# Optimization experiments

Hardware: AMD Instinct MI355X
Metric: run time of the kernel (lower is better)

## Reference

```python
import jax, jax.numpy as jnp
import numpy as np

N = 2          # batch (upsample scale for sample i is i+1, shapes chosen so no crop occurs)
C = 512        # channels for both branches
TH = TW = 256  # target H,W taken from pts_feats[0]
IMG_SIZES = [128, 64, 32, 16, 8]  # 5-level FPN
BN_EPS = 1e-5


def setup_inputs() -> dict:
    key = jax.random.key(0)
    ks = jax.random.split(key, 24)
    inp = {}
    for l, s in enumerate(IMG_SIZES):
        inp[f'img_feat{l}'] = jax.random.normal(ks[l], (N, C, s, s), jnp.float32)
    inp['pts_feat0'] = jax.random.normal(ks[5], (N, C, TH, TW), jnp.float32)
    # 1x1 conv + BN params (eval-mode BN with running stats)
    inp['img_w'] = jax.random.normal(ks[6], (C, C), jnp.float32) * 0.02
    inp['img_b'] = jax.random.normal(ks[7], (C,), jnp.float32) * 0.02
    inp['img_gamma'] = jnp.ones((C,), jnp.float32)
    inp['img_beta'] = jnp.zeros((C,), jnp.float32)
    inp['img_mean'] = jnp.zeros((C,), jnp.float32)
    inp['img_var'] = jax.random.uniform(ks[8], (C,), jnp.float32, 0.5, 1.5)
    inp['pts_w'] = jax.random.normal(ks[9], (C, C), jnp.float32) * 0.02
    inp['pts_b'] = jax.random.normal(ks[10], (C,), jnp.float32) * 0.02
    inp['pts_gamma'] = jnp.ones((C,), jnp.float32)
    inp['pts_beta'] = jnp.zeros((C,), jnp.float32)
    inp['pts_mean'] = jnp.zeros((C,), jnp.float32)
    inp['pts_var'] = jax.random.uniform(ks[11], (C,), jnp.float32, 0.5, 1.5)
    return inp


def _obtain_mlvl(feats, th, tw):
    # Faithful to original: per-sample loop (scale_factor depends on batch index,
    # so each sample has a different static upsampled shape -> Python loop over N=2).
    n = feats[0].shape[0]
    outs = []
    for i in range(n):
        acc = None
        for lvl, f in enumerate(feats):
            x = f[i]  # [C, h, w]
            if lvl > 0:
                s = i + 1  # nearest upsample by batch-index+1 (as in source)
                x = jnp.repeat(jnp.repeat(x, s, axis=1), s, axis=2)
            dh = th - x.shape[1]
            dw = tw - x.shape[2]
            x = jnp.pad(x, ((0, 0), (dh // 2, dh - dh // 2), (dw // 2, dw - dw // 2)), mode='edge')
            acc = x if acc is None else acc + x
        outs.append(acc)
    return jnp.stack(outs, 0)  # [N, C, th, tw]


def _conv_bn_relu(x, w, b, gamma, beta, mean, var):
    # 1x1 conv == channel contraction, then eval-mode BN, then ReLU
    y = jnp.einsum('nchw,oc->nohw', x, w) + b[None, :, None, None]
    scale = gamma / jnp.sqrt(var + BN_EPS)
    y = (y - mean[None, :, None, None]) * scale[None, :, None, None] + beta[None, :, None, None]
    return jax.nn.relu(y)


def reference(img_feat0, img_feat1, img_feat2, img_feat3, img_feat4, pts_feat0,
              img_w, img_b, img_gamma, img_beta, img_mean, img_var,
              pts_w, pts_b, pts_gamma, pts_beta, pts_mean, pts_var):
    th, tw = pts_feat0.shape[2], pts_feat0.shape[3]
    pts_m = _obtain_mlvl([pts_feat0], th, tw)  # pts_levels=1
    pts_pre = _conv_bn_relu(pts_m, pts_w, pts_b, pts_gamma, pts_beta, pts_mean, pts_var)
    img_m = _obtain_mlvl([img_feat0, img_feat1, img_feat2, img_feat3, img_feat4], th, tw)
    img_pre = _conv_bn_relu(img_m, img_w, img_b, img_gamma, img_beta, img_mean, img_var)
    # dropout is identity in eval mode (deterministic reference)
    return jnp.concatenate((img_pre, pts_pre), axis=1)  # [N, 2C, th, tw]
```

## Files before the change

### kernel.cpp

```cpp
#include <hip/hip_runtime.h>

typedef unsigned short u16;
typedef __attribute__((ext_vector_type(8))) short s8frag;
typedef __attribute__((ext_vector_type(4))) float f32x4;

#define GLOAD16(gp, lp)                                                        \
  __builtin_amdgcn_global_load_lds(                                            \
      (const __attribute__((address_space(1))) void*)(gp),                     \
      (__attribute__((address_space(3))) void*)(lp), 16, 0, 0)

__device__ __forceinline__ u16 f2bf(float x) {
  unsigned int u = __float_as_uint(x);
  unsigned int r = (u + 0x7fffu + ((u >> 16) & 1u)) >> 16;
  return (u16)r;
}

__global__ __launch_bounds__(256) void prep_w(
    const float* __restrict__ wi, const float* __restrict__ bi,
    const float* __restrict__ gi, const float* __restrict__ bei,
    const float* __restrict__ mi, const float* __restrict__ vi,
    const float* __restrict__ wp, const float* __restrict__ bp,
    const float* __restrict__ gp, const float* __restrict__ bep,
    const float* __restrict__ mp, const float* __restrict__ vp,
    u16* __restrict__ wout_i, float* __restrict__ bias_i,
    u16* __restrict__ wout_p, float* __restrict__ bias_p) {
  int gidx = blockIdx.x * 256 + threadIdx.x;
  int branch = gidx >> 18;
  int idx = gidx & ((1 << 18) - 1);
  int o = idx >> 9, c = idx & 511;
  const float* w = branch ? wp : wi;
  const float* b = branch ? bp : bi;
  const float* g = branch ? gp : gi;
  const float* be = branch ? bep : bei;
  const float* mn = branch ? mp : mi;
  const float* vr = branch ? vp : vi;
  u16* wo = branch ? wout_p : wout_i;
  float* bo = branch ? bias_p : bias_i;
  float scale = g[o] * rsqrtf(vr[o] + 1e-5f);
  wo[idx] = f2bf(w[idx] * scale);
  if (c == 0) bo[o] = scale * (b[o] - mn[o]) + be[o];
}

__global__ __launch_bounds__(256) void build_b(
    const float* __restrict__ f0, const float* __restrict__ f1,
    const float* __restrict__ f2, const float* __restrict__ f3,
    const float* __restrict__ f4, const float* __restrict__ pts,
    u16* __restrict__ Bimg, u16* __restrict__ Bpts) {
  __shared__ float tile[64][65];
  int t = threadIdx.x;
  int wblk = blockIdx.x;
  int h = blockIdx.y;
  int z = blockIdx.z;
  bool is_img = z < 16;
  int zz = is_img ? z : z - 16;
  int n = zz >> 3;
  int cblk = zz & 7;
  int cbase = cblk * 64;

  if (is_img) {
    int wl = t & 63, w = wblk * 64 + wl;
    const float* feats[5] = {f0, f1, f2, f3, f4};
    const int S[5] = {128, 64, 32, 16, 8};
    int off[5];
#pragma unroll
    for (int l = 0; l < 5; ++l) {
      int s = S[l];
      int scale = (n == 1 && l > 0) ? 2 : 1;
      int u = s * scale, pad = (256 - u) >> 1;
      int ih = h - pad; ih = ih < 0 ? 0 : (ih > u - 1 ? u - 1 : ih); ih /= scale;
      int iw = w - pad; iw = iw < 0 ? 0 : (iw > u - 1 ? u - 1 : iw); iw /= scale;
      off[l] = ih * s + iw;
    }
    for (int cs = 0; cs < 16; ++cs) {
      int cl = cs * 4 + (t >> 6);
      int c = cbase + cl;
      float acc = 0.f;
#pragma unroll
      for (int l = 0; l < 5; ++l) {
        int s = S[l];
        acc += feats[l][(long)(n * 512 + c) * s * s + off[l]];
      }
      tile[cl][wl] = acc;
    }
  } else {
    int wq = t & 15;
    int cl0 = t >> 4;
#pragma unroll
    for (int j = 0; j < 4; ++j) {
      int cl = cl0 + j * 16;
      int c = cbase + cl;
      float4 v = *(const float4*)&pts[((long)(n * 512 + c) * 256 + h) * 256 +
                                      wblk * 64 + wq * 4];
      tile[cl][wq * 4 + 0] = v.x;
      tile[cl][wq * 4 + 1] = v.y;
      tile[cl][wq * 4 + 2] = v.z;
      tile[cl][wq * 4 + 3] = v.w;
    }
  }
  __syncthreads();

  u16* dst = is_img ? Bimg : Bpts;
  long hwb = (long)h * 256 + wblk * 64;
#pragma unroll
  for (int half = 0; half < 2; ++half) {
    int c0 = (t & 7) * 8;
    int wl2 = half * 32 + (t >> 3);
    u16 p[8];
#pragma unroll
    for (int j = 0; j < 8; ++j) p[j] = f2bf(tile[c0 + j][wl2]);
    long di = ((long)n * 65536 + hwb + wl2) * 512 + cbase + c0;
    *(uint4*)(dst + di) = *(const uint4*)p;
  }
}

__global__ __launch_bounds__(1024, 1) void gemm_fused(
    const u16* __restrict__ Aimg, const u16* __restrict__ Apts,
    const u16* __restrict__ Bimg, const u16* __restrict__ Bpts,
    const float* __restrict__ biasImg, const float* __restrict__ biasPts,
    float* __restrict__ out) {
  int br = blockIdx.z;
  const u16* A = br ? Apts : Aimg;
  const u16* B = br ? Bpts : Bimg;
  const float* bias = br ? biasPts : biasImg;

  int s = blockIdx.x;
  int w = (s & 7) * 128 + (s >> 3);
  int rt = w & 1;
  int ct = w >> 1;
  int n = ct >> 8;
  int colbase = (ct & 255) * 256;
  const u16* Bn = B + ((long)n * 65536) * 512;

  __shared__ u16 As[3][256 * 32];
  __shared__ u16 Bs[3][256 * 32];

  int t = threadIdx.x;
  int wave = t >> 6, lane = t & 63;
  int wr = wave >> 2, wc = wave & 3;
  int lrow = lane & 15;
  int q = lane >> 4;

  f32x4 acc[4][4] = {};

#define STAGE(buf, kt_)                                                       \
  {                                                                           \
    int kk_ = (kt_) * 32;                                                     \
    int row = t >> 2, kp = t & 3;                                             \
    int sw = (row >> 1) & 3;                                                  \
    GLOAD16(A + ((long)(rt * 256 + row) * 512 + kk_ + ((kp ^ sw) * 8)),       \
            &As[buf][(t) * 8]);                                               \
    GLOAD16(Bn + ((long)(colbase + row) * 512 + kk_ + ((kp ^ sw) * 8)),       \
            &Bs[buf][(t) * 8]);                                               \
  }

  STAGE(0, 0);
  STAGE(1, 1);
  asm volatile("s_waitcnt vmcnt(2)" ::: "memory");
  __builtin_amdgcn_s_barrier();

#pragma unroll 1
  for (int kt = 0; kt < 16; ++kt) {
    int cur = kt % 3;
    s8frag a[4], b[4];
#pragma unroll
    for (int m = 0; m < 4; ++m) {
      int r = wr * 64 + m * 16 + lrow;
      a[m] = *(const s8frag*)&As[cur][r * 32 + ((q ^ ((r >> 1) & 3)) * 8)];
    }
#pragma unroll
    for (int nn = 0; nn < 4; ++nn) {
      int r = wc * 64 + nn * 16 + lrow;
      b[nn] = *(const s8frag*)&Bs[cur][r * 32 + ((q ^ ((r >> 1) & 3)) * 8)];
    }
    if (kt < 14) STAGE((kt + 2) % 3, kt + 2);
    __builtin_amdgcn_s_setprio(1);
#pragma unroll
    for (int m = 0; m < 4; ++m)
#pragma unroll
      for (int nn = 0; nn < 4; ++nn)
        acc[m][nn] =
            __builtin_amdgcn_mfma_f32_16x16x32_bf16(a[m], b[nn], acc[m][nn], 0, 0, 0);
    __builtin_amdgcn_s_setprio(0);
    if (kt < 15) {
      if (kt < 14)
        asm volatile("s_waitcnt vmcnt(2)" ::: "memory");
      else
        asm volatile("s_waitcnt vmcnt(0)" ::: "memory");
      __builtin_amdgcn_s_barrier();
    }
  }
#undef STAGE

  long outbase = ((long)n * 1024 + br * 512) * 65536;
#pragma unroll
  for (int m = 0; m < 4; ++m) {
    int o0 = rt * 256 + wr * 64 + m * 16 + q * 4;
#pragma unroll
    for (int nn = 0; nn < 4; ++nn) {
      int hw = colbase + wc * 64 + nn * 16 + lrow;
#pragma unroll
      for (int j = 0; j < 4; ++j) {
        int o = o0 + j;
        float v = acc[m][nn][j] + bias[o];
        v = v > 0.f ? v : 0.f;
        out[outbase + (long)o * 65536 + hw] = v;
      }
    }
  }
}

extern "C" void kernel_launch(void* const* d_in, const int* in_sizes, int n_in,
                              void* d_out, int out_size, void* d_ws,
                              size_t ws_size, hipStream_t stream) {
  (void)in_sizes; (void)n_in; (void)out_size; (void)ws_size;
  const float* f0 = (const float*)d_in[0];
  const float* f1 = (const float*)d_in[1];
  const float* f2 = (const float*)d_in[2];
  const float* f3 = (const float*)d_in[3];
  const float* f4 = (const float*)d_in[4];
  const float* pts = (const float*)d_in[5];
  const float* img_w = (const float*)d_in[6];
  const float* img_b = (const float*)d_in[7];
  const float* img_gamma = (const float*)d_in[8];
  const float* img_beta = (const float*)d_in[9];
  const float* img_mean = (const float*)d_in[10];
  const float* img_var = (const float*)d_in[11];
  const float* pts_w = (const float*)d_in[12];
  const float* pts_b = (const float*)d_in[13];
  const float* pts_gamma = (const float*)d_in[14];
  const float* pts_beta = (const float*)d_in[15];
  const float* pts_mean = (const float*)d_in[16];
  const float* pts_var = (const float*)d_in[17];

  char* ws = (char*)d_ws;
  u16* wA_img = (u16*)ws;
  u16* wA_pts = wA_img + 512 * 512;
  float* bias_img = (float*)(ws + (1u << 20));
  float* bias_pts = bias_img + 512;
  u16* Bimg = (u16*)(ws + (2u << 20));
  u16* Bpts = Bimg + (size_t)2 * 65536 * 512;

  prep_w<<<2048, 256, 0, stream>>>(img_w, img_b, img_gamma, img_beta, img_mean,
                                   img_var, pts_w, pts_b, pts_gamma, pts_beta,
                                   pts_mean, pts_var, wA_img, bias_img, wA_pts,
                                   bias_pts);
  build_b<<<dim3(4, 256, 32), 256, 0, stream>>>(f0, f1, f2, f3, f4, pts, Bimg,
                                                Bpts);
  gemm_fused<<<dim3(1024, 1, 2), 1024, 0, stream>>>(
      wA_img, wA_pts, Bimg, Bpts, bias_img, bias_pts, (float*)d_out);
}
```

Measured before the change: 462.5 us.

## Deepen LDS pipeline to four stages and stage epilogue through LDS

The GEMM K-loop moves from triple to quadruple buffering, prefetching three tiles ahead with adjusted vmcnt waits, to hide more global-load latency. The epilogue now transposes each wave's accumulator fragment through padded shared memory so every output row is written as 64 contiguous floats per wave. Before, stores were scattered four floats per lane. This raises LDS use to 128 KB per block and adds an extra barrier plus LDS round trips in the epilogue.

```diff
diff --git a/kernel.cpp b/kernel.cpp
--- a/kernel.cpp
+++ b/kernel.cpp
@@ -131,8 +131,8 @@
   int colbase = (ct & 255) * 256;
   const u16* Bn = B + ((long)n * 65536) * 512;
 
-  __shared__ u16 As[3][256 * 32];
-  __shared__ u16 Bs[3][256 * 32];
+  __shared__ u16 As[4][256 * 32];
+  __shared__ u16 Bs[4][256 * 32];
 
   int t = threadIdx.x;
   int wave = t >> 6, lane = t & 63;
@@ -155,12 +155,13 @@
 
   STAGE(0, 0);
   STAGE(1, 1);
-  asm volatile("s_waitcnt vmcnt(2)" ::: "memory");
+  STAGE(2, 2);
+  asm volatile("s_waitcnt vmcnt(4)" ::: "memory");
   __builtin_amdgcn_s_barrier();
 
 #pragma unroll 1
   for (int kt = 0; kt < 16; ++kt) {
-    int cur = kt % 3;
+    int cur = kt & 3;
     s8frag a[4], b[4];
 #pragma unroll
     for (int m = 0; m < 4; ++m) {
@@ -172,7 +173,7 @@
       int r = wc * 64 + nn * 16 + lrow;
       b[nn] = *(const s8frag*)&Bs[cur][r * 32 + ((q ^ ((r >> 1) & 3)) * 8)];
     }
-    if (kt < 14) STAGE((kt + 2) % 3, kt + 2);
+    if (kt < 13) STAGE((kt + 3) & 3, kt + 3);
     __builtin_amdgcn_s_setprio(1);
 #pragma unroll
     for (int m = 0; m < 4; ++m)
@@ -182,7 +183,9 @@
             __builtin_amdgcn_mfma_f32_16x16x32_bf16(a[m], b[nn], acc[m][nn], 0, 0, 0);
     __builtin_amdgcn_s_setprio(0);
     if (kt < 15) {
-      if (kt < 14)
+      if (kt <= 12)
+        asm volatile("s_waitcnt vmcnt(4)" ::: "memory");
+      else if (kt == 13)
         asm volatile("s_waitcnt vmcnt(2)" ::: "memory");
       else
         asm volatile("s_waitcnt vmcnt(0)" ::: "memory");
@@ -191,21 +194,26 @@
   }
 #undef STAGE
 
+  __builtin_amdgcn_s_barrier();
+  float* epi = (float*)((char*)&As[0][0] + (size_t)wave * 4160);
   long outbase = ((long)n * 1024 + br * 512) * 65536;
-#pragma unroll
+  int hwb = colbase + wc * 64;
+#pragma unroll 1
   for (int m = 0; m < 4; ++m) {
-    int o0 = rt * 256 + wr * 64 + m * 16 + q * 4;
-#pragma unroll
-    for (int nn = 0; nn < 4; ++nn) {
-      int hw = colbase + wc * 64 + nn * 16 + lrow;
-#pragma unroll
-      for (int j = 0; j < 4; ++j) {
-        int o = o0 + j;
-        float v = acc[m][nn][j] + bias[o];
-        v = v > 0.f ? v : 0.f;
-        out[outbase + (long)o * 65536 + hw] = v;
-      }
-    }
+#pragma unroll
+    for (int nn = 0; nn < 4; ++nn)
+#pragma unroll
+      for (int j = 0; j < 4; ++j)
+        epi[(q * 4 + j) * 65 + nn * 16 + lrow] = acc[m][nn][j];
+    asm volatile("s_waitcnt lgkmcnt(0)" ::: "memory");
+#pragma unroll
+    for (int r = 0; r < 16; ++r) {
+      int o = rt * 256 + wr * 64 + m * 16 + r;
+      float v = epi[r * 65 + lane] + bias[o];
+      v = v > 0.f ? v : 0.f;
+      out[outbase + (long)o * 65536 + hwb + lane] = v;
+    }
+    asm volatile("s_waitcnt lgkmcnt(0)" ::: "memory");
   }
 }
 
```

After: 640.1 us. +38.4%, slower.
